# Kernel optimization log

Hardware: AMD Instinct MI355X
Metric: run time of the kernel (lower is better)

Reference implementation:

```python
import jax, jax.numpy as jnp
import numpy as np

B, S, D = 64, 500, 1024  # batch, seq_len, input_dim == hidden_dim
MAX_POS = 500

def _lin(k, din, dout):
    k1, k2 = jax.random.split(k)
    s = 1.0 / np.sqrt(din)
    W = jax.random.uniform(k1, (din, dout), jnp.float32, -s, s)
    b = jax.random.uniform(k2, (dout,), jnp.float32, -s, s)
    return W, b

def setup_inputs() -> dict:
    key = jax.random.key(0)
    ks = jax.random.split(key, 12)
    x = jax.random.normal(ks[0], (B, S, D), jnp.float32)
    pos_emb = jax.random.normal(ks[1], (MAX_POS, D), jnp.float32)
    Wq_fw, bq_fw = _lin(ks[2], D, D)
    Wk_fw, bk_fw = _lin(ks[3], D, D)
    Wv_fw, bv_fw = _lin(ks[4], D, D)
    Wq_bw, bq_bw = _lin(ks[5], D, D)
    Wk_bw, bk_bw = _lin(ks[6], D, D)
    Wv_bw, bv_bw = _lin(ks[7], D, D)
    Wg_fw, bg_fw = _lin(ks[8], 2 * D, D)
    Wg_bw, bg_bw = _lin(ks[9], 2 * D, D)
    W2, b2 = _lin(ks[10], 2 * D, 2 * D)
    W1, b1 = _lin(ks[11], 2 * D, 2 * D)
    return dict(x=x, pos_emb=pos_emb,
                Wq_fw=Wq_fw, bq_fw=bq_fw, Wk_fw=Wk_fw, bk_fw=bk_fw, Wv_fw=Wv_fw, bv_fw=bv_fw,
                Wq_bw=Wq_bw, bq_bw=bq_bw, Wk_bw=Wk_bw, bk_bw=bk_bw, Wv_bw=Wv_bw, bv_bw=bv_bw,
                Wg_fw=Wg_fw, bg_fw=bg_fw, Wg_bw=Wg_bw, bg_bw=bg_bw,
                W2=W2, b2=b2, W1=W1, b1=b1)

def _attn(q, k, v, mask, d):
    # q,k,v: [B,S,D]; mask: [S,S] bool (True = keep)
    scores = jnp.einsum('bqd,bkd->bqk', q, k) / jnp.sqrt(jnp.float32(d))
    scores = jnp.where(mask[None], scores, jnp.float32(-1e9))
    probs = jax.nn.softmax(scores, axis=-1)  # dropout is identity in eval
    return jnp.einsum('bqk,bkd->bqd', probs, v)

def reference(x, pos_emb, Wq_fw, bq_fw, Wk_fw, bk_fw, Wv_fw, bv_fw,
              Wq_bw, bq_bw, Wk_bw, bk_bw, Wv_bw, bv_bw,
              Wg_fw, bg_fw, Wg_bw, bg_bw, W2, b2, W1, b1):
    b, s, d = x.shape
    H = x + pos_emb[:s][None]  # [B,S,D]
    tri = jnp.tril(jnp.ones((s, s), dtype=bool))
    H_mF = _attn(H @ Wq_fw + bq_fw, H @ Wk_fw + bk_fw, H @ Wv_fw + bv_fw, tri, d)
    H_mB = _attn(H @ Wq_bw + bq_bw, H @ Wk_bw + bk_bw, H @ Wv_bw + bv_bw, tri.T, d)
    G_fw = jax.nn.sigmoid(jnp.concatenate([H, H_mF], -1) @ Wg_fw + bg_fw)
    C_F = G_fw * H + (1.0 - G_fw) * H_mF
    G_bw = jax.nn.sigmoid(jnp.concatenate([H, H_mB], -1) @ Wg_bw + bg_bw)
    C_B = G_bw * H + (1.0 - G_bw) * H_mB
    C_i = jnp.concatenate([C_F, C_B], -1)  # [B,S,2D]
    activ = jax.nn.sigmoid(C_i @ W2 + b2)
    scores = activ @ W1 + b1
    attn_w = jax.nn.softmax(scores, axis=1)  # softmax over seq dim
    utt_vec = jnp.sum(attn_w * C_i, axis=1)  # [B,2D]
    return utt_vec, C_i
```

## Files before the change

### kernel.cpp

```cpp
#include <hip/hip_runtime.h>

typedef __bf16 bf16;
typedef __bf16 bf16x4 __attribute__((ext_vector_type(4)));
typedef __bf16 bf16x8 __attribute__((ext_vector_type(8)));
typedef float  f32x4  __attribute__((ext_vector_type(4)));
typedef unsigned int u32;

#define GLD_LDS16(gsrc, ldst) \
  __builtin_amdgcn_global_load_lds((const __attribute__((address_space(1))) u32*)(gsrc), \
                                   (__attribute__((address_space(3))) u32*)(ldst), 16, 0, 0)

static __device__ __forceinline__ float sigmoidf_(float x) { return 1.0f / (1.0f + expf(-x)); }

__global__ void fill_guard(float* __restrict__ utt, float v) {
  int i = blockIdx.x * 256 + threadIdx.x;
  if (i < 131072) utt[i] = v;
}

__global__ void add_pos_bf(const float* __restrict__ x, const float* __restrict__ pos,
                           bf16* __restrict__ H) {
  size_t i = ((size_t)blockIdx.x * 256 + threadIdx.x) * 4;
  if (i >= 32768000ull) return;
  int d = (int)(i & 1023);
  int s = (int)((i >> 10) % 500);
  float4 xv = *(const float4*)(x + i);
  float4 pv = *(const float4*)(pos + (size_t)s * 1024 + d);
  bf16x4 o;
  o[0] = (bf16)(xv.x + pv.x); o[1] = (bf16)(xv.y + pv.y);
  o[2] = (bf16)(xv.z + pv.z); o[3] = (bf16)(xv.w + pv.w);
  *(bf16x4*)(H + i) = o;
}

__global__ void wtrans(const float* __restrict__ src, bf16* __restrict__ dst, int R, int C) {
  __shared__ float tile[32][33];
  int c0 = blockIdx.x * 32, r0 = blockIdx.y * 32;
  int tr = threadIdx.x >> 5, tc = threadIdx.x & 31;
#pragma unroll
  for (int i = 0; i < 4; ++i)
    tile[tr + i * 8][tc] = src[(size_t)(r0 + tr + i * 8) * C + c0 + tc];
  __syncthreads();
#pragma unroll
  for (int i = 0; i < 4; ++i) {
    int rr = tr + i * 8;
    dst[(size_t)(c0 + rr) * R + r0 + tc] = (bf16)tile[tc][rr];
  }
}

template <int EPI, typename TC>
__global__ __launch_bounds__(512, 2) void mgemm256(
    const bf16* __restrict__ A, const bf16* __restrict__ A2, int ksplit,
    const bf16* __restrict__ Bt, const float* __restrict__ bias, TC* __restrict__ C,
    bf16* __restrict__ Cbf,
    int M, int N, int K, int lda, int ldb, int ldc, int c_off, float scale,
    const bf16* __restrict__ Gh, const bf16* __restrict__ Gm) {
  extern __shared__ char sm[];
  const int t = threadIdx.x;

  const int gx = gridDim.x;
  const int nwg = gx * gridDim.y;
  const int orig = blockIdx.y * gx + blockIdx.x;
  const int qq = nwg >> 3, r8 = nwg & 7;
  const int xcd = orig & 7, lo = orig >> 3;
  const int wg = (xcd < r8 ? xcd * (qq + 1) : r8 * (qq + 1) + (xcd - r8) * qq) + lo;
  const int m0 = (wg / gx) * 256, n0 = (wg % gx) * 256;

  const int lane = t & 63;
  const int w = t >> 6, wr = w >> 2, wc = w & 3;
  const int srow = t >> 3, schunk = t & 7, scol = schunk * 8;
  const int hi16 = (lane >> 4) << 4;

  f32x4 acc[8][4];
#pragma unroll
  for (int i = 0; i < 8; ++i)
#pragma unroll
    for (int j = 0; j < 4; ++j)
#pragma unroll
      for (int c = 0; c < 4; ++c) acc[i][j][c] = 0.0f;

#define STAGE_Q(tt, cb, h) do {                                                     \
    const int k0s_ = (tt) * 64;                                                     \
    char* lb_ = sm + (cb) * 65536 + ((h) < 2 ? 0 : 32768);                          \
    _Pragma("unroll")                                                               \
    for (int i_ = 0; i_ < 2; ++i_) {                                                \
      int rl_ = ((h) & 1) * 128 + i_ * 64 + srow;                                   \
      int cx_ = scol ^ ((rl_ & 7) << 3);                                            \
      if ((h) < 2) {                                                                \
        int rg_ = m0 + rl_; rg_ = rg_ < M ? rg_ : M - 1;                            \
        const bf16* s_ = (k0s_ < ksplit)                                            \
            ? A  + (size_t)rg_ * lda + k0s_ + cx_                                   \
            : A2 + (size_t)rg_ * lda + (k0s_ - ksplit) + cx_;                       \
        GLD_LDS16(s_, lb_ + rl_ * 128 + schunk * 16);                               \
      } else {                                                                      \
        int rg_ = n0 + rl_; rg_ = rg_ < N ? rg_ : N - 1;                            \
        GLD_LDS16(Bt + (size_t)rg_ * ldb + k0s_ + cx_, lb_ + rl_ * 128 + schunk * 16); \
      }                                                                             \
    }                                                                               \
  } while (0)

  const int NT = K >> 6;
  STAGE_Q(0, 0, 0); STAGE_Q(0, 0, 1); STAGE_Q(0, 0, 2); STAGE_Q(0, 0, 3);

  for (int t0 = 0; t0 < NT; ++t0) {
    const int cur = t0 & 1;
    char* smA = sm + cur * 65536;
    char* smB = smA + 32768;
    const bool pf = (t0 + 1 < NT);

    if (pf) {
      STAGE_Q(t0 + 1, cur ^ 1, 0);
      asm volatile("s_waitcnt vmcnt(2)" ::: "memory");
    } else {
      asm volatile("s_waitcnt vmcnt(0)" ::: "memory");
    }
    __builtin_amdgcn_s_barrier();

    bf16x8 bfr[4][2];
#pragma unroll
    for (int fc = 0; fc < 4; ++fc)
#pragma unroll
      for (int ks = 0; ks < 2; ++ks) {
        int rb = wc * 64 + fc * 16 + (lane & 15);
        int byb = (ks * 64 + hi16) ^ ((rb & 7) << 4);
        bfr[fc][ks] = *(const bf16x8*)(smB + rb * 128 + byb);
      }

#pragma unroll
    for (int p = 0; p < 4; ++p) {
      if (p > 0 && pf) STAGE_Q(t0 + 1, cur ^ 1, p);
      bf16x8 afr[2][2];
#pragma unroll
      for (int e = 0; e < 2; ++e)
#pragma unroll
        for (int ks = 0; ks < 2; ++ks) {
          int ra = wr * 128 + (2 * p + e) * 16 + (lane & 15);
          int bya = (ks * 64 + hi16) ^ ((ra & 7) << 4);
          afr[e][ks] = *(const bf16x8*)(smA + ra * 128 + bya);
        }
      if (p > 0) __builtin_amdgcn_s_barrier();
      __builtin_amdgcn_s_setprio(1);
#pragma unroll
      for (int e = 0; e < 2; ++e)
#pragma unroll
        for (int fc = 0; fc < 4; ++fc)
#pragma unroll
          for (int ks = 0; ks < 2; ++ks)
            acc[2 * p + e][fc] = __builtin_amdgcn_mfma_f32_16x16x32_bf16(
                afr[e][ks], bfr[fc][ks], acc[2 * p + e][fc], 0, 0, 0);
      __builtin_amdgcn_s_setprio(0);
      __builtin_amdgcn_s_barrier();
    }
  }
#undef STAGE_Q

#pragma unroll
  for (int fr = 0; fr < 8; ++fr) {
#pragma unroll
    for (int j4 = 0; j4 < 4; ++j4) {
      int m = m0 + wr * 128 + fr * 16 + ((lane >> 4) << 2) + j4;
      if (m >= M) continue;
#pragma unroll
      for (int fc = 0; fc < 4; ++fc) {
        int n = n0 + wc * 64 + fc * 16 + (lane & 15);
        if (n >= N) continue;
        float v = acc[fr][fc][j4] * scale;
        if (bias) v += bias[n];
        if (EPI == 1) v = sigmoidf_(v);
        if (EPI == 2) {
          float g = sigmoidf_(v);
          float h  = (float)Gh[(size_t)m * 1024 + n];
          float hm = (float)Gm[(size_t)m * 1024 + n];
          v = g * h + (1.0f - g) * hm;
        }
        if (EPI == 3) {
          unsigned b = (unsigned)m / 500u;
          unsigned s = (unsigned)m - b * 500u;
          C[(size_t)b * 524288 + (size_t)n * 512 + s] = (TC)v;
        } else {
          C[(size_t)m * ldc + c_off + n] = (TC)v;
          if (EPI == 2 && Cbf) Cbf[(size_t)m * 2048 + c_off + n] = (bf16)v;
        }
      }
    }
  }
}

template <int EPI, typename TC>
__global__ __launch_bounds__(256, 2) void mgemm(
    const bf16* __restrict__ A, const bf16* __restrict__ A2, int ksplit,
    const bf16* __restrict__ Bt, const float* __restrict__ bias, TC* __restrict__ C,
    int M, int N, int K, int lda, int ldb, int ldc, int c_off, float scale,
    long long sA, long long sB, long long sC,
    const bf16* __restrict__ Gh, const bf16* __restrict__ Gm) {
  __shared__ __align__(16) char sm[16384];
  const int t = threadIdx.x;
  const long long bz = blockIdx.z;
  A += bz * sA; A2 += bz * sA; Bt += bz * sB; C += bz * sC;
  const int m0 = blockIdx.y * 128, n0 = blockIdx.x * 128;

  f32x4 acc[4][4];
#pragma unroll
  for (int i = 0; i < 4; ++i)
#pragma unroll
    for (int j = 0; j < 4; ++j)
#pragma unroll
      for (int c = 0; c < 4; ++c) acc[i][j][c] = 0.0f;

  const int lane = t & 63;
  const int wv = t >> 6, wm = (wv >> 1) * 64, wn = (wv & 1) * 64;
  const int lr = lane & 15, lkb = (lane >> 4) * 16;
  const int rr = t >> 2, cc = (t & 3) * 8;

  for (int k0 = 0; k0 < K; k0 += 32) {
    const bf16* Ak = (k0 < ksplit) ? (A + k0) : (A2 + (k0 - ksplit));
    const bf16* Bk = Bt + k0;
#pragma unroll
    for (int j = 0; j < 2; ++j) {
      int ra = m0 + j * 64 + rr; ra = ra < M ? ra : M - 1;
      GLD_LDS16(Ak + (size_t)ra * lda + cc, sm + j * 4096 + t * 16);
      int rb = n0 + j * 64 + rr; rb = rb < N ? rb : N - 1;
      GLD_LDS16(Bk + (size_t)rb * ldb + cc, sm + 8192 + j * 4096 + t * 16);
    }
    asm volatile("s_waitcnt vmcnt(0)" ::: "memory");
    __syncthreads();

    bf16x8 av[4], bv[4];
#pragma unroll
    for (int i = 0; i < 4; ++i) {
      av[i] = *(const bf16x8*)(sm + (wm + i * 16 + lr) * 64 + lkb);
      bv[i] = *(const bf16x8*)(sm + 8192 + (wn + i * 16 + lr) * 64 + lkb);
    }
#pragma unroll
    for (int i = 0; i < 4; ++i)
#pragma unroll
      for (int j = 0; j < 4; ++j)
        acc[i][j] = __builtin_amdgcn_mfma_f32_16x16x32_bf16(av[i], bv[j], acc[i][j], 0, 0, 0);
    __syncthreads();
  }

#pragma unroll
  for (int i = 0; i < 4; ++i) {
#pragma unroll
    for (int j4 = 0; j4 < 4; ++j4) {
      int m = m0 + wm + i * 16 + (lane >> 4) * 4 + j4;
      if (m >= M) continue;
#pragma unroll
      for (int j = 0; j < 4; ++j) {
        int n = n0 + wn + j * 16 + (lane & 15);
        if (n >= N) continue;
        float v = acc[i][j][j4] * scale;
        if (bias) v += bias[n];
        C[(size_t)m * ldc + c_off + n] = (TC)v;
      }
    }
  }
}

__global__ void attn_softmax_w(const float* __restrict__ S, bf16* __restrict__ P, int fw) {
  int row = blockIdx.x * 4 + (threadIdx.x >> 6);
  int lane = threadIdx.x & 63;
  int q = row % 500;
  const float* Srow = S + (size_t)row * 512;
  bf16* Prow = P + (size_t)row * 512;
  int klo = fw ? 0 : q;
  int khi = fw ? q : 499;

  float xv[8];
  float m = -1e30f;
#pragma unroll
  for (int i = 0; i < 8; ++i) {
    int k = lane + i * 64;
    bool valid = (k >= klo) & (k <= khi);
    float v = valid ? Srow[k] : -1e30f;
    xv[i] = v;
    m = fmaxf(m, v);
  }
#pragma unroll
  for (int off = 32; off > 0; off >>= 1) m = fmaxf(m, __shfl_xor(m, off, 64));
  float e[8];
  float sum = 0.0f;
#pragma unroll
  for (int i = 0; i < 8; ++i) {
    e[i] = (xv[i] > -1e29f) ? expf(xv[i] - m) : 0.0f;
    sum += e[i];
  }
#pragma unroll
  for (int off = 32; off > 0; off >>= 1) sum += __shfl_xor(sum, off, 64);
  float inv = 1.0f / sum;
#pragma unroll
  for (int i = 0; i < 8; ++i) Prow[lane + i * 64] = (bf16)(e[i] * inv);
}

__global__ void final_reduce_chunk(const float* __restrict__ s2, const float* __restrict__ Ci,
                                   float* __restrict__ utt) {
  int c = blockIdx.x * 256 + threadIdx.x;
  int b = blockIdx.y;
  if (c >= 2048) return;
  float m = -1e30f, sum = 0.0f, acc = 0.0f;
  for (int s = 0; s < 500; ++s) {
    size_t idx = ((size_t)(b * 500 + s)) * 2048 + c;
    float xx = s2[idx];
    float ci = Ci[idx];
    float mn = fmaxf(m, xx);
    float corr = expf(m - mn);
    float e = expf(xx - mn);
    sum = sum * corr + e;
    acc = acc * corr + e * ci;
    m = mn;
  }
  utt[(size_t)b * 2048 + c] = acc / sum;
}

extern "C" void kernel_launch(void* const* d_in, const int* in_sizes, int n_in,
                              void* d_out, int out_size, void* d_ws, size_t ws_size,
                              hipStream_t stream) {
  (void)in_sizes; (void)n_in; (void)out_size;
  float* utt = (float*)d_out;
  float* Ci  = (float*)d_out + 131072;

  const float* x     = (const float*)d_in[0];
  const float* pos   = (const float*)d_in[1];
  const float* Wq_fw = (const float*)d_in[2];  const float* bq_fw = (const float*)d_in[3];
  const float* Wk_fw = (const float*)d_in[4];  const float* bk_fw = (const float*)d_in[5];
  const float* Wv_fw = (const float*)d_in[6];  const float* bv_fw = (const float*)d_in[7];
  const float* Wq_bw = (const float*)d_in[8];  const float* bq_bw = (const float*)d_in[9];
  const float* Wk_bw = (const float*)d_in[10]; const float* bk_bw = (const float*)d_in[11];
  const float* Wv_bw = (const float*)d_in[12]; const float* bv_bw = (const float*)d_in[13];
  const float* Wg_fw = (const float*)d_in[14]; const float* bg_fw = (const float*)d_in[15];
  const float* Wg_bw = (const float*)d_in[16]; const float* bg_bw = (const float*)d_in[17];
  const float* W2    = (const float*)d_in[18]; const float* b2    = (const float*)d_in[19];
  const float* W1    = (const float*)d_in[20]; const float* b1    = (const float*)d_in[21];

  const size_t WS_BYTES = 465305600ull;
  if (ws_size < WS_BYTES) { fill_guard<<<512, 256, 0, stream>>>(utt, 500.0f); return; }

  char* wsb = (char*)d_ws;
  bf16*  Hbf  = (bf16*)(wsb);
  bf16*  Qb   = (bf16*)(wsb + 65536000);
  bf16*  Kb   = (bf16*)(wsb + 131072000);
  bf16*  Vt   = (bf16*)(wsb + 196608000);
  float* Sb   = (float*)(wsb + 263716864);
  bf16*  Hmb  = (bf16*)(wsb + 263716864);
  bf16*  Pb   = (bf16*)(wsb + 329252864);
  char*  wts  = wsb + 362020864;
  bf16* WqF = (bf16*)(wts);             bf16* WkF = (bf16*)(wts + 2097152);
  bf16* WvF = (bf16*)(wts + 4194304);   bf16* WqB = (bf16*)(wts + 6291456);
  bf16* WkB = (bf16*)(wts + 8388608);   bf16* WvB = (bf16*)(wts + 10485760);
  bf16* WgF = (bf16*)(wts + 12582912);  bf16* WgB = (bf16*)(wts + 16777216);
  bf16* W2t = (bf16*)(wts + 20971520);  bf16* W1t = (bf16*)(wts + 29360128);
  bf16*  Cibf  = (bf16*)(wsb + 399769600);
  bf16*  activ = (bf16*)(wsb + 131072000);
  float* s2b   = (float*)(wsb);

  hipFuncSetAttribute(reinterpret_cast<const void*>(&mgemm256<0, bf16>),
                      hipFuncAttributeMaxDynamicSharedMemorySize, 131072);
  hipFuncSetAttribute(reinterpret_cast<const void*>(&mgemm256<3, bf16>),
                      hipFuncAttributeMaxDynamicSharedMemorySize, 131072);
  hipFuncSetAttribute(reinterpret_cast<const void*>(&mgemm256<2, float>),
                      hipFuncAttributeMaxDynamicSharedMemorySize, 131072);
  hipFuncSetAttribute(reinterpret_cast<const void*>(&mgemm256<1, bf16>),
                      hipFuncAttributeMaxDynamicSharedMemorySize, 131072);
  hipFuncSetAttribute(reinterpret_cast<const void*>(&mgemm256<0, float>),
                      hipFuncAttributeMaxDynamicSharedMemorySize, 131072);

  add_pos_bf<<<32000, 256, 0, stream>>>(x, pos, Hbf);

  struct WT { const float* s; bf16* d; int R, C; } wt[10] = {
      {Wq_fw, WqF, 1024, 1024}, {Wk_fw, WkF, 1024, 1024}, {Wv_fw, WvF, 1024, 1024},
      {Wq_bw, WqB, 1024, 1024}, {Wk_bw, WkB, 1024, 1024}, {Wv_bw, WvB, 1024, 1024},
      {Wg_fw, WgF, 2048, 1024}, {Wg_bw, WgB, 2048, 1024},
      {W2,    W2t, 2048, 2048}, {W1,    W1t, 2048, 2048}};
  for (int i = 0; i < 10; ++i)
    wtrans<<<dim3(wt[i].C / 32, wt[i].R / 32), 256, 0, stream>>>(wt[i].s, wt[i].d, wt[i].R, wt[i].C);

  const int BIG = 1 << 30;
  for (int dir = 0; dir < 2; ++dir) {
    const bf16* WqT = dir ? WqB : WqF;  const float* bq = dir ? bq_bw : bq_fw;
    const bf16* WkT = dir ? WkB : WkF;  const float* bk = dir ? bk_bw : bk_fw;
    const bf16* WvT = dir ? WvB : WvF;  const float* bv = dir ? bv_bw : bv_fw;
    const bf16* WgT = dir ? WgB : WgF;  const float* bg = dir ? bg_bw : bg_fw;

    mgemm256<0, bf16><<<dim3(4, 125), 512, 131072, stream>>>(
        Hbf, Hbf, BIG, WqT, bq, Qb, nullptr, 32000, 1024, 1024, 1024, 1024, 1024, 0, 1.0f,
        nullptr, nullptr);
    mgemm256<0, bf16><<<dim3(4, 125), 512, 131072, stream>>>(
        Hbf, Hbf, BIG, WkT, bk, Kb, nullptr, 32000, 1024, 1024, 1024, 1024, 1024, 0, 1.0f,
        nullptr, nullptr);
    mgemm256<3, bf16><<<dim3(4, 125), 512, 131072, stream>>>(
        Hbf, Hbf, BIG, WvT, bv, Vt, nullptr, 32000, 1024, 1024, 1024, 1024, 512, 0, 1.0f,
        nullptr, nullptr);
    mgemm<0, float><<<dim3(4, 4, 64), 256, 0, stream>>>(
        Qb, Qb, BIG, Kb, nullptr, Sb, 500, 500, 1024, 1024, 1024, 512, 0, 0.03125f,
        512000, 512000, 256000, nullptr, nullptr);
    attn_softmax_w<<<8000, 256, 0, stream>>>(Sb, Pb, dir == 0 ? 1 : 0);
    mgemm<0, bf16><<<dim3(8, 4, 64), 256, 0, stream>>>(
        Pb, Pb, BIG, Vt, nullptr, Hmb, 500, 1024, 512, 512, 512, 1024, 0, 1.0f,
        256000, 524288, 512000, nullptr, nullptr);
    mgemm256<2, float><<<dim3(8, 125), 512, 131072, stream>>>(
        Hbf, Hmb, 1024, WgT, bg, Ci, Cibf, 32000, 1024, 2048, 1024, 2048, 2048,
        dir == 0 ? 0 : 1024, 1.0f, Hbf, Hmb);
  }

  mgemm256<1, bf16><<<dim3(8, 125), 512, 131072, stream>>>(
      Cibf, Cibf, BIG, W2t, b2, activ, nullptr, 32000, 2048, 2048, 2048, 2048, 2048, 0, 1.0f,
      nullptr, nullptr);

  for (int c0 = 0; c0 < 2; ++c0) {
    mgemm256<0, float><<<dim3(8, 63), 512, 131072, stream>>>(
        activ + (size_t)c0 * 16000 * 2048, activ, BIG, W1t, b1, s2b, nullptr,
        16000, 2048, 2048, 2048, 2048, 2048, 0, 1.0f, nullptr, nullptr);
    final_reduce_chunk<<<dim3(8, 32), 256, 0, stream>>>(
        s2b, Ci + (size_t)c0 * 32 * 500 * 2048, utt + (size_t)c0 * 32 * 2048);
  }
}
```

Before: 2.856 ms.

## Move QKV projections to 128x128 GEMM with XCD remap; restructure 256 GEMM pipeline

The Q, K and V projections now run on the smaller 128x128 mgemm kernel with an 8x250 grid instead of the 256-tile LDS-pipelined kernel. mgemm gains an XCD-aware workgroup remapping so that consecutive tiles land on the same XCD for L2 reuse. The V-transpose epilogue moves into mgemm. The 256 kernel's main loop now waits on all outstanding loads up front, double-buffers A fragments in registers, and drops the per-phase barriers. Removing those barriers may risk races between the async LDS prefetch into the other buffer and reads of the current one, and the full vmcnt(0) wait serialises the load/compute overlap.

Result: no change. 2.827 ms (-1.0%).

```diff
diff --git a/kernel.cpp b/kernel.cpp
--- a/kernel.cpp
+++ b/kernel.cpp
@@ -106,12 +106,7 @@
     char* smB = smA + 32768;
     const bool pf = (t0 + 1 < NT);
 
-    if (pf) {
-      STAGE_Q(t0 + 1, cur ^ 1, 0);
-      asm volatile("s_waitcnt vmcnt(2)" ::: "memory");
-    } else {
-      asm volatile("s_waitcnt vmcnt(0)" ::: "memory");
-    }
+    asm volatile("s_waitcnt vmcnt(0)" ::: "memory");
     __builtin_amdgcn_s_barrier();
 
     bf16x8 bfr[4][2];
@@ -123,20 +118,29 @@
         int byb = (ks * 64 + hi16) ^ ((rb & 7) << 4);
         bfr[fc][ks] = *(const bf16x8*)(smB + rb * 128 + byb);
       }
+    bf16x8 afr[2][2][2];
+#pragma unroll
+    for (int e = 0; e < 2; ++e)
+#pragma unroll
+      for (int ks = 0; ks < 2; ++ks) {
+        int ra = wr * 128 + e * 16 + (lane & 15);
+        int bya = (ks * 64 + hi16) ^ ((ra & 7) << 4);
+        afr[0][e][ks] = *(const bf16x8*)(smA + ra * 128 + bya);
+      }
 
 #pragma unroll
     for (int p = 0; p < 4; ++p) {
-      if (p > 0 && pf) STAGE_Q(t0 + 1, cur ^ 1, p);
-      bf16x8 afr[2][2];
-#pragma unroll
-      for (int e = 0; e < 2; ++e)
-#pragma unroll
-        for (int ks = 0; ks < 2; ++ks) {
-          int ra = wr * 128 + (2 * p + e) * 16 + (lane & 15);
-          int bya = (ks * 64 + hi16) ^ ((ra & 7) << 4);
-          afr[e][ks] = *(const bf16x8*)(smA + ra * 128 + bya);
-        }
-      if (p > 0) __builtin_amdgcn_s_barrier();
+      if (pf) STAGE_Q(t0 + 1, cur ^ 1, p);
+      if (p < 3) {
+#pragma unroll
+        for (int e = 0; e < 2; ++e)
+#pragma unroll
+          for (int ks = 0; ks < 2; ++ks) {
+            int ra = wr * 128 + (2 * (p + 1) + e) * 16 + (lane & 15);
+            int bya = (ks * 64 + hi16) ^ ((ra & 7) << 4);
+            afr[(p + 1) & 1][e][ks] = *(const bf16x8*)(smA + ra * 128 + bya);
+          }
+      }
       __builtin_amdgcn_s_setprio(1);
 #pragma unroll
       for (int e = 0; e < 2; ++e)
@@ -145,9 +149,8 @@
 #pragma unroll
           for (int ks = 0; ks < 2; ++ks)
             acc[2 * p + e][fc] = __builtin_amdgcn_mfma_f32_16x16x32_bf16(
-                afr[e][ks], bfr[fc][ks], acc[2 * p + e][fc], 0, 0, 0);
+                afr[p & 1][e][ks], bfr[fc][ks], acc[2 * p + e][fc], 0, 0, 0);
       __builtin_amdgcn_s_setprio(0);
-      __builtin_amdgcn_s_barrier();
     }
   }
 #undef STAGE_Q
@@ -171,14 +174,8 @@
           float hm = (float)Gm[(size_t)m * 1024 + n];
           v = g * h + (1.0f - g) * hm;
         }
-        if (EPI == 3) {
-          unsigned b = (unsigned)m / 500u;
-          unsigned s = (unsigned)m - b * 500u;
-          C[(size_t)b * 524288 + (size_t)n * 512 + s] = (TC)v;
-        } else {
-          C[(size_t)m * ldc + c_off + n] = (TC)v;
-          if (EPI == 2 && Cbf) Cbf[(size_t)m * 2048 + c_off + n] = (bf16)v;
-        }
+        C[(size_t)m * ldc + c_off + n] = (TC)v;
+        if (EPI == 2 && Cbf) Cbf[(size_t)m * 2048 + c_off + n] = (bf16)v;
       }
     }
   }
@@ -189,13 +186,19 @@
     const bf16* __restrict__ A, const bf16* __restrict__ A2, int ksplit,
     const bf16* __restrict__ Bt, const float* __restrict__ bias, TC* __restrict__ C,
     int M, int N, int K, int lda, int ldb, int ldc, int c_off, float scale,
-    long long sA, long long sB, long long sC,
-    const bf16* __restrict__ Gh, const bf16* __restrict__ Gm) {
+    long long sA, long long sB, long long sC) {
   __shared__ __align__(16) char sm[16384];
   const int t = threadIdx.x;
   const long long bz = blockIdx.z;
   A += bz * sA; A2 += bz * sA; Bt += bz * sB; C += bz * sC;
-  const int m0 = blockIdx.y * 128, n0 = blockIdx.x * 128;
+
+  const int gx = gridDim.x;
+  const int nwg = gx * gridDim.y;
+  const int orig = blockIdx.y * gx + blockIdx.x;
+  const int qq = nwg >> 3, r8 = nwg & 7;
+  const int xcd = orig & 7, lo = orig >> 3;
+  const int wg = (xcd < r8 ? xcd * (qq + 1) : r8 * (qq + 1) + (xcd - r8) * qq) + lo;
+  const int m0 = (wg / gx) * 128, n0 = (wg % gx) * 128;
 
   f32x4 acc[4][4];
 #pragma unroll
@@ -249,7 +252,13 @@
         if (n >= N) continue;
         float v = acc[i][j][j4] * scale;
         if (bias) v += bias[n];
-        C[(size_t)m * ldc + c_off + n] = (TC)v;
+        if (EPI == 3) {
+          unsigned b = (unsigned)m / 500u;
+          unsigned s = (unsigned)m - b * 500u;
+          C[(size_t)b * 524288 + (size_t)n * 512 + s] = (TC)v;
+        } else {
+          C[(size_t)m * ldc + c_off + n] = (TC)v;
+        }
       }
     }
   }
@@ -351,10 +360,6 @@
   bf16*  activ = (bf16*)(wsb + 131072000);
   float* s2b   = (float*)(wsb);
 
-  hipFuncSetAttribute(reinterpret_cast<const void*>(&mgemm256<0, bf16>),
-                      hipFuncAttributeMaxDynamicSharedMemorySize, 131072);
-  hipFuncSetAttribute(reinterpret_cast<const void*>(&mgemm256<3, bf16>),
-                      hipFuncAttributeMaxDynamicSharedMemorySize, 131072);
   hipFuncSetAttribute(reinterpret_cast<const void*>(&mgemm256<2, float>),
                       hipFuncAttributeMaxDynamicSharedMemorySize, 131072);
   hipFuncSetAttribute(reinterpret_cast<const void*>(&mgemm256<1, bf16>),
@@ -379,22 +384,19 @@
     const bf16* WvT = dir ? WvB : WvF;  const float* bv = dir ? bv_bw : bv_fw;
     const bf16* WgT = dir ? WgB : WgF;  const float* bg = dir ? bg_bw : bg_fw;
 
-    mgemm256<0, bf16><<<dim3(4, 125), 512, 131072, stream>>>(
-        Hbf, Hbf, BIG, WqT, bq, Qb, nullptr, 32000, 1024, 1024, 1024, 1024, 1024, 0, 1.0f,
-        nullptr, nullptr);
-    mgemm256<0, bf16><<<dim3(4, 125), 512, 131072, stream>>>(
-        Hbf, Hbf, BIG, WkT, bk, Kb, nullptr, 32000, 1024, 1024, 1024, 1024, 1024, 0, 1.0f,
-        nullptr, nullptr);
-    mgemm256<3, bf16><<<dim3(4, 125), 512, 131072, stream>>>(
-        Hbf, Hbf, BIG, WvT, bv, Vt, nullptr, 32000, 1024, 1024, 1024, 1024, 512, 0, 1.0f,
-        nullptr, nullptr);
+    mgemm<0, bf16><<<dim3(8, 250, 1), 256, 0, stream>>>(
+        Hbf, Hbf, BIG, WqT, bq, Qb, 32000, 1024, 1024, 1024, 1024, 1024, 0, 1.0f, 0, 0, 0);
+    mgemm<0, bf16><<<dim3(8, 250, 1), 256, 0, stream>>>(
+        Hbf, Hbf, BIG, WkT, bk, Kb, 32000, 1024, 1024, 1024, 1024, 1024, 0, 1.0f, 0, 0, 0);
+    mgemm<3, bf16><<<dim3(8, 250, 1), 256, 0, stream>>>(
+        Hbf, Hbf, BIG, WvT, bv, Vt, 32000, 1024, 1024, 1024, 1024, 512, 0, 1.0f, 0, 0, 0);
     mgemm<0, float><<<dim3(4, 4, 64), 256, 0, stream>>>(
         Qb, Qb, BIG, Kb, nullptr, Sb, 500, 500, 1024, 1024, 1024, 512, 0, 0.03125f,
-        512000, 512000, 256000, nullptr, nullptr);
+        512000, 512000, 256000);
     attn_softmax_w<<<8000, 256, 0, stream>>>(Sb, Pb, dir == 0 ? 1 : 0);
     mgemm<0, bf16><<<dim3(8, 4, 64), 256, 0, stream>>>(
         Pb, Pb, BIG, Vt, nullptr, Hmb, 500, 1024, 512, 512, 512, 1024, 0, 1.0f,
-        256000, 524288, 512000, nullptr, nullptr);
+        256000, 524288, 512000);
     mgemm256<2, float><<<dim3(8, 125), 512, 131072, stream>>>(
         Hbf, Hmb, 1024, WgT, bg, Ci, Cibf, 32000, 1024, 2048, 1024, 2048, 2048,
         dir == 0 ? 0 : 1024, 1.0f, Hbf, Hmb);
```
